# Performance work log

Hardware: AMD Instinct MI355X
Metric: run time of the kernel (lower is better)

Reference implementation:

```python
import jax, jax.numpy as jnp
from jax import lax
import numpy as np

# Bit order convention: pulse index 0 = MSB (sign bit), index 31 = LSB of mantissa.
SHIFTS = jnp.arange(31, -1, -1, dtype=jnp.uint32)  # [32]


def f32_to_pulses(x):
    """float32 [...] -> pulse bits [..., 32] in {0.,1.}"""
    u = lax.bitcast_convert_type(x.astype(jnp.float32), jnp.uint32)
    return ((u[..., None] >> SHIFTS) & jnp.uint32(1)).astype(jnp.float32)


def pulses_to_f32(p):
    """pulse bits [..., 32] -> float32 [...]"""
    bits = (p > 0.5).astype(jnp.uint32)
    u = jnp.sum(bits << SHIFTS, axis=-1).astype(jnp.uint32)
    return lax.bitcast_convert_type(u, jnp.float32)


def setup_inputs() -> dict:
    key = jax.random.key(0)
    kx, kw = jax.random.split(key)
    B, IN, OUT = 256, 1024, 1024
    x_f = jax.random.normal(kx, (B, IN), dtype=jnp.float32)
    w_f = jax.random.normal(kw, (OUT, IN), dtype=jnp.float32) * (1.0 / np.sqrt(IN))
    return {"x": f32_to_pulses(x_f), "weight_pulse": f32_to_pulses(w_f)}


def reference(x, weight_pulse):
    # Decode pulses to IEEE-754 FP32 values (exact: the spiking multiplier/adder
    # implement bit-exact FP32 arithmetic).
    xf = pulses_to_f32(x)              # [B, in]
    wf = pulses_to_f32(weight_pulse)   # [out, in]
    prods = xf[..., None, :] * wf      # [B, out, in]
    # SequentialAccumulator: strictly left-to-right FP32 accumulation (bit-exact
    # deterministic order), expressed as a scan over the in_features axis.
    acc0 = jnp.zeros(prods.shape[:-1], dtype=jnp.float32)  # [B, out]
    acc, _ = lax.scan(lambda a, p: (a + p, None), acc0, jnp.moveaxis(prods, -1, 0))
    # Re-encode the FP32 result to output pulses [B, out, 32].
    return f32_to_pulses(acc)
```

## Files before the change

kernel.cpp:

```cpp
#include <hip/hip_runtime.h>
#include <cstdint>

#define BATCH 256
#define INF   1024
#define OUTF  1024

__device__ __forceinline__ uint32_t assemble_bits(const float4* __restrict__ p4) {
    uint32_t u = 0;
#pragma unroll
    for (int j = 0; j < 8; ++j) {
        float4 v = p4[j];
        int sh = 31 - j * 4;
        u |= (v.x > 0.5f ? 1u : 0u) << sh;
        u |= (v.y > 0.5f ? 1u : 0u) << (sh - 1);
        u |= (v.z > 0.5f ? 1u : 0u) << (sh - 2);
        u |= (v.w > 0.5f ? 1u : 0u) << (sh - 3);
    }
    return u;
}

__global__ __launch_bounds__(256) void decode_pulses(
    const float* __restrict__ pulses, float* __restrict__ out, int n) {
    int i = blockIdx.x * blockDim.x + threadIdx.x;
    if (i >= n) return;
    const float4* p4 = reinterpret_cast<const float4*>(pulses) + (size_t)i * 8;
    out[i] = __uint_as_float(assemble_bits(p4));
}

__global__ __launch_bounds__(512) void decode_w_transpose(
    const float* __restrict__ pulses,
    float* __restrict__ wT)
{
    __shared__ float tile[64][65];
    const int o0 = blockIdx.x * 64;
    const int k0 = blockIdx.y * 64;
    const int t  = threadIdx.x;

    const int o_loc  = t >> 3;
    const int k_base = t & 7;
    const float4* src = reinterpret_cast<const float4*>(pulses)
                        + ((size_t)(o0 + o_loc) * INF + k0 + k_base) * 8;
#pragma unroll
    for (int j = 0; j < 8; ++j) {
        tile[o_loc][k_base + 8 * j] = __uint_as_float(assemble_bits(src + (size_t)(8 * j) * 8));
    }
    __syncthreads();

    const int col = t & 63;
    const int w   = t >> 6;
#pragma unroll
    for (int j2 = 0; j2 < 8; ++j2) {
        int krow = j2 * 8 + w;
        wT[(size_t)(k0 + krow) * OUTF + o0 + col] = tile[col][krow];
    }
}

__global__ __launch_bounds__(256) void gemm_encode(
    const float* __restrict__ xf,
    const float* __restrict__ wT,
    float* __restrict__ out)
{
#pragma clang fp contract(off)
    __shared__ float w_s[64 * 64];
    __shared__ float x_s[8][64];
    const int tx = threadIdx.x, ty = threadIdx.y;
    const int t  = ty * 64 + tx;
    const int o0 = blockIdx.x * 64;
    const int b0 = blockIdx.y * 8;

    const int wrow = t >> 4;
    const int wseg = t & 15;

    float acc0 = 0.0f, acc1 = 0.0f;

    for (int kt = 0; kt < 16; ++kt) {
        const int k0 = kt * 64;
        __syncthreads();
        {
#pragma unroll
            for (int h = 0; h < 4; ++h) {
                float4 v = *reinterpret_cast<const float4*>(
                    wT + (size_t)(k0 + wrow + 16 * h) * OUTF + o0 + wseg * 4);
                *reinterpret_cast<float4*>(&w_s[(size_t)(t + 256 * h) * 4]) = v;
            }
        }
        if (t < 128) {
            int xr = t >> 4, xs = t & 15;
            float4 v = *reinterpret_cast<const float4*>(
                xf + (size_t)(b0 + xr) * INF + k0 + xs * 4);
            *reinterpret_cast<float4*>(&x_s[xr][xs * 4]) = v;
        }
        __syncthreads();

        const float* wcol  = w_s + tx;
        const float* xrow0 = x_s[ty * 2];
        const float* xrow1 = x_s[ty * 2 + 1];
#pragma unroll
        for (int k4 = 0; k4 < 16; ++k4) {
            float4 xa = *reinterpret_cast<const float4*>(xrow0 + k4 * 4);
            float4 xb = *reinterpret_cast<const float4*>(xrow1 + k4 * 4);
            float w0 = wcol[(k4 * 4 + 0) * 64];
            float w1 = wcol[(k4 * 4 + 1) * 64];
            float w2 = wcol[(k4 * 4 + 2) * 64];
            float w3 = wcol[(k4 * 4 + 3) * 64];
            acc0 = acc0 + xa.x * w0;
            acc0 = acc0 + xa.y * w1;
            acc0 = acc0 + xa.z * w2;
            acc0 = acc0 + xa.w * w3;
            acc1 = acc1 + xb.x * w0;
            acc1 = acc1 + xb.y * w1;
            acc1 = acc1 + xb.z * w2;
            acc1 = acc1 + xb.w * w3;
        }
    }

    const int o = o0 + tx;
    float accs[2] = {acc0, acc1};
#pragma unroll
    for (int q = 0; q < 2; ++q) {
        uint32_t u = __float_as_uint(accs[q]);
        float4* dst = reinterpret_cast<float4*>(out)
                      + ((size_t)(b0 + ty * 2 + q) * OUTF + o) * 8;
#pragma unroll
        for (int j = 0; j < 8; ++j) {
            int sh = 31 - j * 4;
            dst[j] = make_float4((float)((u >> sh) & 1u),
                                 (float)((u >> (sh - 1)) & 1u),
                                 (float)((u >> (sh - 2)) & 1u),
                                 (float)((u >> (sh - 3)) & 1u));
        }
    }
}

extern "C" void kernel_launch(void* const* d_in, const int* in_sizes, int n_in,
                              void* d_out, int out_size, void* d_ws, size_t ws_size,
                              hipStream_t stream) {
    const float* x_pulses = (const float*)d_in[0];
    const float* w_pulses = (const float*)d_in[1];
    float* out = (float*)d_out;

    float* xf = (float*)d_ws;
    float* wT = xf + (size_t)BATCH * INF;

    {
        int n = BATCH * INF;
        decode_pulses<<<(n + 255) / 256, 256, 0, stream>>>(x_pulses, xf, n);
    }
    {
        decode_w_transpose<<<dim3(16, 16), 512, 0, stream>>>(w_pulses, wT);
    }
    {
        dim3 grid(OUTF / 64, BATCH / 8);
        dim3 block(64, 4);
        gemm_encode<<<grid, block, 0, stream>>>(xf, wT, out);
    }
}
```

Before: 279.8 us.

## Drop weight transpose kernel and prefetch next k-tile into registers in GEMM

The separate decode-and-transpose kernel for weights is replaced by the plain decode kernel writing row-major weights. The GEMM now loads weight rows directly and transposes them while storing to shared memory. It also register-prefetches the next k-tile's weights and activations while computing the current one, so global loads overlap compute. The trade-offs are that scalar transposed shared stores may cause bank conflicts, and global weight loads become strided by row (each thread reads its own row).

```diff
diff --git a/kernel.cpp b/kernel.cpp
--- a/kernel.cpp
+++ b/kernel.cpp
@@ -27,37 +27,9 @@
     out[i] = __uint_as_float(assemble_bits(p4));
 }
 
-__global__ __launch_bounds__(512) void decode_w_transpose(
-    const float* __restrict__ pulses,
-    float* __restrict__ wT)
-{
-    __shared__ float tile[64][65];
-    const int o0 = blockIdx.x * 64;
-    const int k0 = blockIdx.y * 64;
-    const int t  = threadIdx.x;
-
-    const int o_loc  = t >> 3;
-    const int k_base = t & 7;
-    const float4* src = reinterpret_cast<const float4*>(pulses)
-                        + ((size_t)(o0 + o_loc) * INF + k0 + k_base) * 8;
-#pragma unroll
-    for (int j = 0; j < 8; ++j) {
-        tile[o_loc][k_base + 8 * j] = __uint_as_float(assemble_bits(src + (size_t)(8 * j) * 8));
-    }
-    __syncthreads();
-
-    const int col = t & 63;
-    const int w   = t >> 6;
-#pragma unroll
-    for (int j2 = 0; j2 < 8; ++j2) {
-        int krow = j2 * 8 + w;
-        wT[(size_t)(k0 + krow) * OUTF + o0 + col] = tile[col][krow];
-    }
-}
-
 __global__ __launch_bounds__(256) void gemm_encode(
     const float* __restrict__ xf,
-    const float* __restrict__ wT,
+    const float* __restrict__ wf,
     float* __restrict__ out)
 {
 #pragma clang fp contract(off)
@@ -68,29 +40,42 @@
     const int o0 = blockIdx.x * 64;
     const int b0 = blockIdx.y * 8;
 
-    const int wrow = t >> 4;
-    const int wseg = t & 15;
+    const int o_loc = t & 63;
+    const int seg0  = t >> 6;
+    const float* __restrict__ wbase = wf + (size_t)(o0 + o_loc) * INF;
+    const int xr = t >> 4, xs = t & 15;
+
+    float4 wreg[4];
+    float4 xreg;
+
+#pragma unroll
+    for (int h = 0; h < 4; ++h)
+        wreg[h] = *reinterpret_cast<const float4*>(wbase + (seg0 + 4 * h) * 4);
+    if (t < 128)
+        xreg = *reinterpret_cast<const float4*>(xf + (size_t)(b0 + xr) * INF + xs * 4);
+#pragma unroll
+    for (int h = 0; h < 4; ++h) {
+        const int s = seg0 + 4 * h;
+        w_s[(s * 4 + 0) * 64 + o_loc] = wreg[h].x;
+        w_s[(s * 4 + 1) * 64 + o_loc] = wreg[h].y;
+        w_s[(s * 4 + 2) * 64 + o_loc] = wreg[h].z;
+        w_s[(s * 4 + 3) * 64 + o_loc] = wreg[h].w;
+    }
+    if (t < 128)
+        *reinterpret_cast<float4*>(&x_s[xr][xs * 4]) = xreg;
+    __syncthreads();
 
     float acc0 = 0.0f, acc1 = 0.0f;
 
     for (int kt = 0; kt < 16; ++kt) {
-        const int k0 = kt * 64;
-        __syncthreads();
-        {
+        if (kt < 15) {
+            const int k0 = (kt + 1) * 64;
 #pragma unroll
-            for (int h = 0; h < 4; ++h) {
-                float4 v = *reinterpret_cast<const float4*>(
-                    wT + (size_t)(k0 + wrow + 16 * h) * OUTF + o0 + wseg * 4);
-                *reinterpret_cast<float4*>(&w_s[(size_t)(t + 256 * h) * 4]) = v;
-            }
+            for (int h = 0; h < 4; ++h)
+                wreg[h] = *reinterpret_cast<const float4*>(wbase + k0 + (seg0 + 4 * h) * 4);
+            if (t < 128)
+                xreg = *reinterpret_cast<const float4*>(xf + (size_t)(b0 + xr) * INF + k0 + xs * 4);
         }
-        if (t < 128) {
-            int xr = t >> 4, xs = t & 15;
-            float4 v = *reinterpret_cast<const float4*>(
-                xf + (size_t)(b0 + xr) * INF + k0 + xs * 4);
-            *reinterpret_cast<float4*>(&x_s[xr][xs * 4]) = v;
-        }
-        __syncthreads();
 
         const float* wcol  = w_s + tx;
         const float* xrow0 = x_s[ty * 2];
@@ -111,6 +96,21 @@
             acc1 = acc1 + xb.y * w1;
             acc1 = acc1 + xb.z * w2;
             acc1 = acc1 + xb.w * w3;
+        }
+        __syncthreads();
+
+        if (kt < 15) {
+#pragma unroll
+            for (int h = 0; h < 4; ++h) {
+                const int s = seg0 + 4 * h;
+                w_s[(s * 4 + 0) * 64 + o_loc] = wreg[h].x;
+                w_s[(s * 4 + 1) * 64 + o_loc] = wreg[h].y;
+                w_s[(s * 4 + 2) * 64 + o_loc] = wreg[h].z;
+                w_s[(s * 4 + 3) * 64 + o_loc] = wreg[h].w;
+            }
+            if (t < 128)
+                *reinterpret_cast<float4*>(&x_s[xr][xs * 4]) = xreg;
+            __syncthreads();
         }
     }
 
@@ -140,18 +140,19 @@
     float* out = (float*)d_out;
 
     float* xf = (float*)d_ws;
-    float* wT = xf + (size_t)BATCH * INF;
+    float* wf = xf + (size_t)BATCH * INF;
 
     {
         int n = BATCH * INF;
         decode_pulses<<<(n + 255) / 256, 256, 0, stream>>>(x_pulses, xf, n);
     }
     {
-        decode_w_transpose<<<dim3(16, 16), 512, 0, stream>>>(w_pulses, wT);
+        int n = OUTF * INF;
+        decode_pulses<<<n / 256, 256, 0, stream>>>(w_pulses, wf, n);
     }
     {
         dim3 grid(OUTF / 64, BATCH / 8);
         dim3 block(64, 4);
-        gemm_encode<<<grid, block, 0, stream>>>(xf, wT, out);
+        gemm_encode<<<grid, block, 0, stream>>>(xf, wf, out);
     }
 }
```

Measured after the change: 251.7 us. 10.1% less time.
